# Optimization experiments

Measured on AMD Instinct MI355X. Metric: run time of the kernel, lower is better.

Reference implementation:

```python
import jax, jax.numpy as jnp
import numpy as np

DIM = 384
HEADS = 8
HEAD_DIM = DIM // HEADS
TEM_LEN = 400
SCALE = HEAD_DIM ** -0.5


def setup_inputs() -> dict:
    key = jax.random.key(0)
    ks = jax.random.split(key, 12)
    B, Lq, Lkv = 16, 1024, 1424
    inp = {
        'tem_mask': jax.random.normal(ks[0], (B, TEM_LEN, DIM), jnp.float32),
        'search_mask': jax.random.normal(ks[1], (B, Lkv - TEM_LEN, DIM), jnp.float32),
        'q': jax.random.normal(ks[2], (B, Lq, DIM), jnp.float32),
        'kv': jax.random.normal(ks[3], (B, Lkv, DIM), jnp.float32),
        'attn_pos': jax.random.normal(ks[4], (1, HEADS, Lq, Lkv), jnp.float32),
        # learned params (attn_pos_encoding_only=True: q, fused kv, proj)
        'q_w': jax.random.normal(ks[5], (DIM, DIM), jnp.float32) * 0.02,
        'q_b': jnp.zeros((DIM,), jnp.float32),
        'kv_w': jax.random.normal(ks[6], (2 * DIM, DIM), jnp.float32) * 0.02,
        'kv_b': jnp.zeros((2 * DIM,), jnp.float32),
        'proj_w': jax.random.normal(ks[7], (DIM, DIM), jnp.float32) * 0.02,
        'proj_b': jnp.zeros((DIM,), jnp.float32),
    }
    return inp


def reference(tem_mask, search_mask, q, kv, attn_pos, q_w, q_b, kv_w, kv_b, proj_w, proj_b):
    B, Lq, C = q.shape
    Lkv = kv.shape[1]
    # projections
    qh = (q @ q_w.T + q_b).reshape(B, Lq, HEADS, HEAD_DIM).transpose(0, 2, 1, 3)  # (B,H,Lq,hd)
    kvp = kv @ kv_w.T + kv_b                                                      # (B,Lkv,2C)
    k = kvp[..., :C]
    v = kvp[..., C:]
    # additive masks on v before head split (template tokens first, then search)
    v = jnp.concatenate([v[:, :TEM_LEN] + tem_mask, v[:, TEM_LEN:] + search_mask], axis=1)
    kh = k.reshape(B, Lkv, HEADS, HEAD_DIM).transpose(0, 2, 1, 3)  # (B,H,Lkv,hd)
    vh = v.reshape(B, Lkv, HEADS, HEAD_DIM).transpose(0, 2, 1, 3)  # (B,H,Lkv,hd)
    # scaled scores + untied positional bias, softmax over keys
    attn = jnp.einsum('bhqd,bhkd->bhqk', qh, kh) * SCALE + attn_pos
    attn = jax.nn.softmax(attn, axis=-1)
    x = jnp.einsum('bhqk,bhkd->bhqd', attn, vh)
    x = x.transpose(0, 2, 1, 3).reshape(B, Lq, C)
    return x @ proj_w.T + proj_b
```

## Files before the change

kernel.cpp:

```cpp
#include <hip/hip_runtime.h>
#include <stdint.h>

#define NB 16
#define NH 8
#define LQ 1024
#define LKV 1424
#define LKVP 1472
#define DIMC 384
#define NKVT 23
#define TEM 400
#define QSCALE 0.20823509f
#define LOG2E_F 1.4426950408889634f

typedef __attribute__((ext_vector_type(4))) float f32x4;
typedef __attribute__((ext_vector_type(8))) short bf16x8;
typedef __attribute__((ext_vector_type(4))) unsigned short us4;
typedef __attribute__((ext_vector_type(2))) unsigned int u32x2;
typedef __attribute__((ext_vector_type(4))) unsigned int u32x4;

__device__ __forceinline__ unsigned short f2b(float f) {
  unsigned int u = __builtin_bit_cast(unsigned int, f);
  u += 0x7fffu + ((u >> 16) & 1u);
  return (unsigned short)(u >> 16);
}

__device__ __forceinline__ void gload_lds16(const void* gsrc, void* ldst) {
  __builtin_amdgcn_global_load_lds(
      (const __attribute__((address_space(1))) void*)gsrc,
      (__attribute__((address_space(3))) void*)ldst, 16, 0, 0);
}

__global__ __launch_bounds__(256) void prep_all(
    const float* __restrict__ q, const float* __restrict__ kv,
    const float* __restrict__ qw, const float* __restrict__ kvw,
    const float* __restrict__ pw, const float* __restrict__ pos,
    unsigned short* __restrict__ qb, unsigned short* __restrict__ kvb,
    unsigned short* __restrict__ qwb, unsigned short* __restrict__ kvwb,
    unsigned short* __restrict__ pwb, unsigned short* __restrict__ Qp,
    unsigned short* __restrict__ Kp, unsigned short* __restrict__ Vt,
    unsigned short* __restrict__ posb) {
  __shared__ float lds[4][1024];
  const int bid = blockIdx.x;
  if (bid < 7632) {
    int i = bid * 256 + threadIdx.x;
    const float* src;
    unsigned short* dst;
    if (i < 16384 * 48) { src = q; dst = qb; }
    else if (i < 39168 * 48) { i -= 16384 * 48; src = kv; dst = kvb; }
    else if (i < 39552 * 48) { i -= 39168 * 48; src = qw; dst = qwb; }
    else if (i < 40320 * 48) { i -= 39552 * 48; src = kvw; dst = kvwb; }
    else { i -= 40320 * 48; src = pw; dst = pwb; }
    int row = i / 48, ch = i - row * 48;
    const float* sp = src + (size_t)row * DIMC + ch * 8;
    f32x4 x = *(const f32x4*)sp;
    f32x4 y = *(const f32x4*)(sp + 4);
    bf16x8 o;
    o[0] = (short)f2b(x[0]); o[1] = (short)f2b(x[1]);
    o[2] = (short)f2b(x[2]); o[3] = (short)f2b(x[3]);
    o[4] = (short)f2b(y[0]); o[5] = (short)f2b(y[1]);
    o[6] = (short)f2b(y[2]); o[7] = (short)f2b(y[3]);
    int blk = ch >> 3, c3 = (ch & 7) ^ (row & 7);
    *(bf16x8*)(dst + (size_t)row * DIMC + blk * 64 + c3 * 8) = o;
  } else if (bid < 9024) {
    int i = (bid - 7632) * 256 + threadIdx.x;
    u32x4 z = {0u, 0u, 0u, 0u};
    if (i < 131072) {
      *(u32x4*)(Qp + (size_t)i * 64 + 48) = z;
      *(u32x4*)(Qp + (size_t)i * 64 + 56) = z;
    } else if (i < 131072 + 188416) {
      int r = i - 131072;
      int s = r % LKVP;
      unsigned short* row = Kp + (size_t)r * 64;
      if (s < LKV) {
        *(u32x4*)(row + (6 ^ (s & 7)) * 8) = z;
        *(u32x4*)(row + (7 ^ (s & 7)) * 8) = z;
      } else {
#pragma unroll
        for (int c = 0; c < 64; c += 8) *(u32x4*)(row + c) = z;
      }
    } else if (i < 131072 + 188416 + 36864) {
      int j = i - 319488;
      int row = j / 6, x = 2 + j - (j / 6) * 6;
      int d = row % 48;
      *(u32x4*)(Vt + (size_t)row * LKVP + 1408 + ((x ^ d) & 7) * 8) = z;
    }
  } else {
    const int r = bid - 9024;
    const int q16 = r & 63, h = r >> 6;
    const int wave = threadIdx.x >> 6, lane = threadIdx.x & 63;
    const int l16 = lane & 15, g = lane >> 4;
    float* L = &lds[wave][0];
    for (int t = wave; t < NKVT; t += 4) {
#pragma unroll
      for (int i = 0; i < 4; ++i) {
        const int row = i * 4 + g;
        const int gcol = t * 64 + l16 * 4;
        f32x4 v;
        if (gcol < LKV) {
          v = *(const f32x4*)(pos + ((size_t)h * LQ + q16 * 16 + row) * LKV + gcol);
          v *= LOG2E_F;
        } else {
          f32x4 neg = {-1e30f, -1e30f, -1e30f, -1e30f};
          v = neg;
        }
        *(f32x4*)(L + row * 64 + ((l16 ^ (row & 7)) << 2)) = v;
      }
      unsigned short vals[16];
#pragma unroll
      for (int ni = 0; ni < 4; ++ni) {
        f32x4 wv = *(const f32x4*)(L + l16 * 64 + (((4 * ni + g) ^ (l16 & 7)) << 2));
#pragma unroll
        for (int rr = 0; rr < 4; ++rr) vals[4 * ni + rr] = f2b(wv[rr]);
      }
      unsigned short* op = posb + ((((size_t)h * 64 + q16) * NKVT + t) * 64 + lane) * 16;
      bf16x8 a, b;
#pragma unroll
      for (int k = 0; k < 8; ++k) { a[k] = (short)vals[k]; b[k] = (short)vals[8 + k]; }
      *(bf16x8*)op = a;
      *(bf16x8*)(op + 8) = b;
    }
  }
}

template <int MODE>
__device__ __forceinline__ void proj_body(
    unsigned short* Ash, unsigned short* Bsh, int n0, int m0,
    const unsigned short* __restrict__ A, const unsigned short* __restrict__ Wb,
    const float* __restrict__ bias, const float* __restrict__ tem,
    const float* __restrict__ srch, unsigned short* __restrict__ Oq,
    unsigned short* __restrict__ Ok, unsigned short* __restrict__ Ovt,
    float* __restrict__ Of) {
  const int tid = threadIdx.x;
  const int lane = tid & 63, l16 = lane & 15, g = lane >> 4;
  const int wave = tid >> 6, wm = wave >> 1, wn = wave & 1;

  f32x4 acc[4][4];
#pragma unroll
  for (int i = 0; i < 4; ++i)
#pragma unroll
    for (int j = 0; j < 4; ++j) { f32x4 z = {0.f, 0.f, 0.f, 0.f}; acc[i][j] = z; }

  const char* Abase = (const char*)A + (size_t)m0 * 768;
  const char* Bbase = (const char*)Wb + (size_t)n0 * 768;

  for (int ks = 0; ks < 6; ++ks) {
    __syncthreads();
#pragma unroll
    for (int rnd = 0; rnd < 4; ++rnd) {
      int idx = tid + rnd * 256;
      int row = idx >> 3, chunk = idx & 7;
      gload_lds16(Abase + (size_t)row * 768 + ks * 128 + chunk * 16,
                  (char*)Ash + idx * 16);
    }
#pragma unroll
    for (int rnd = 0; rnd < 4; ++rnd) {
      int idx = tid + rnd * 256;
      int row = idx >> 3, chunk = idx & 7;
      gload_lds16(Bbase + (size_t)row * 768 + ks * 128 + chunk * 16,
                  (char*)Bsh + idx * 16);
    }
    asm volatile("s_waitcnt vmcnt(0)" ::: "memory");
    __syncthreads();
#pragma unroll
    for (int kk = 0; kk < 2; ++kk) {
      bf16x8 a[4], bb[4];
#pragma unroll
      for (int mi = 0; mi < 4; ++mi) {
        int row = wm * 64 + mi * 16 + l16;
        a[mi] = *(const bf16x8*)((char*)Ash + row * 128 + (((g + 4 * kk) ^ (row & 7)) << 4));
      }
#pragma unroll
      for (int ni = 0; ni < 4; ++ni) {
        int row = wn * 64 + ni * 16 + l16;
        bb[ni] = *(const bf16x8*)((char*)Bsh + row * 128 + (((g + 4 * kk) ^ (row & 7)) << 4));
      }
#pragma unroll
      for (int mi = 0; mi < 4; ++mi)
#pragma unroll
        for (int ni = 0; ni < 4; ++ni)
          acc[mi][ni] = __builtin_amdgcn_mfma_f32_16x16x32_bf16(a[mi], bb[ni], acc[mi][ni], 0, 0, 0);
    }
  }

#pragma unroll
  for (int mi = 0; mi < 4; ++mi) {
    const int m_g0 = m0 + wm * 64 + mi * 16 + 4 * g;
#pragma unroll
    for (int ni = 0; ni < 4; ++ni) {
      const int n_g = n0 + wn * 64 + ni * 16 + l16;
      const float bv = bias[n_g];
      if (MODE == 0) {
        const int hh = n_g / 48, d = n_g - hh * 48;
#pragma unroll
        for (int r = 0; r < 4; ++r) {
          const int m_g = m_g0 + r;
          const int b = m_g >> 10, m = m_g & 1023;
          Oq[(((size_t)b * NH + hh) * LQ + m) * 64 + d] = f2b((acc[mi][ni][r] + bv) * QSCALE);
        }
      } else if (MODE == 2) {
#pragma unroll
        for (int r = 0; r < 4; ++r)
          Of[(size_t)(m_g0 + r) * DIMC + n_g] = acc[mi][ni][r] + bv;
      } else {
        const int b = m_g0 / LKV, s0 = m_g0 - b * LKV;
        if (n_g < DIMC) {
          const int hh = n_g / 48, d = n_g - hh * 48;
#pragma unroll
          for (int r = 0; r < 4; ++r) {
            const int s = s0 + r;
            const int dsw = (d & 7) | ((((d >> 3) ^ (s & 7)) & 7) << 3);
            Ok[(((size_t)b * NH + hh) * LKVP + s) * 64 + dsw] = f2b(acc[mi][ni][r] + bv);
          }
        } else {
          const int c = n_g - DIMC, hh = c / 48, d = c - hh * 48;
          const float* mb = (s0 < TEM)
                                ? tem + ((size_t)b * TEM + s0) * DIMC + c
                                : srch + ((size_t)b * (LKV - TEM) + (s0 - TEM)) * DIMC + c;
          const int off = s0 & 63;
          const int soff = (s0 & ~63) | ((((off >> 3) ^ d) & 7) << 3) | (off & 7);
          us4 pk;
#pragma unroll
          for (int r = 0; r < 4; ++r)
            pk[r] = f2b(acc[mi][ni][r] + bv + mb[(size_t)r * DIMC]);
          *(us4*)(Ovt + (((size_t)b * NH + hh) * 48 + d) * LKVP + soff) = pk;
        }
      }
    }
  }
}

__global__ __launch_bounds__(256) void proj_qkv(
    const unsigned short* __restrict__ qb, const unsigned short* __restrict__ qwb,
    const float* __restrict__ q_b, const unsigned short* __restrict__ kvb,
    const unsigned short* __restrict__ kvwb, const float* __restrict__ kv_b,
    const float* __restrict__ tem, const float* __restrict__ srch,
    unsigned short* __restrict__ Qp, unsigned short* __restrict__ Ok,
    unsigned short* __restrict__ Ovt) {
  __shared__ unsigned short Ash[128 * 64];
  __shared__ unsigned short Bsh[128 * 64];
  const int bid = blockIdx.x;
  if (bid < 384) {
    proj_body<0>(Ash, Bsh, (bid % 3) * 128, (bid / 3) * 128, qb, qwb, q_b,
                 nullptr, nullptr, Qp, nullptr, nullptr, nullptr);
  } else {
    const int r = bid - 384;
    proj_body<1>(Ash, Bsh, (r % 6) * 128, (r / 6) * 128, kvb, kvwb, kv_b,
                 tem, srch, nullptr, Ok, Ovt, nullptr);
  }
}

__global__ __launch_bounds__(256) void proj_out(
    const unsigned short* __restrict__ X, const unsigned short* __restrict__ pwb,
    const float* __restrict__ p_b, float* __restrict__ out) {
  __shared__ unsigned short Ash[128 * 64];
  __shared__ unsigned short Bsh[128 * 64];
  proj_body<2>(Ash, Bsh, (blockIdx.x % 3) * 128, (blockIdx.x / 3) * 128, X, pwb, p_b,
               nullptr, nullptr, nullptr, nullptr, nullptr, out);
}

__device__ __forceinline__ void stage_tile(const char* kbase, const char* vbase, int t,
                                           char* kdst, char* vdst, int wave, int lane) {
  const char* ks = kbase + (size_t)t * 8192 + wave * 2048 + lane * 16;
  char* kd = kdst + wave * 2048;
  gload_lds16(ks, kd);
  gload_lds16(ks + 1024, kd + 1024);
  if (wave < 3) {
    const char* vs = vbase + (size_t)(wave * 16 + (lane >> 3)) * (LKVP * 2) +
                     (size_t)t * 128 + (lane & 7) * 16;
    char* vd = vdst + wave * 2048;
    gload_lds16(vs, vd);
    gload_lds16(vs + 8 * (LKVP * 2), vd + 1024);
  }
}

__device__ __forceinline__ float expsum16(f32x4 (&sx)[4]) {
#pragma unroll
  for (int ni = 0; ni < 4; ++ni)
#pragma unroll
    for (int r = 0; r < 4; ++r) sx[ni][r] = exp2f(sx[ni][r]);
  float s0 = (sx[0][0] + sx[0][1]) + (sx[0][2] + sx[0][3]);
  float s1 = (sx[1][0] + sx[1][1]) + (sx[1][2] + sx[1][3]);
  float s2 = (sx[2][0] + sx[2][1]) + (sx[2][2] + sx[2][3]);
  float s3 = (sx[3][0] + sx[3][1]) + (sx[3][2] + sx[3][3]);
  float sum = (s0 + s1) + (s2 + s3);
  sum += __shfl_xor(sum, 16);
  sum += __shfl_xor(sum, 32);
  return sum;
}

__device__ __forceinline__ void packP(const f32x4 (&sx)[4], char* pbase, int swz, int g,
                                      bf16x8& af0, bf16x8& af1) {
#pragma unroll
  for (int ni = 0; ni < 4; ++ni) {
    float e0 = sx[ni][0], e1 = sx[ni][1], e2 = sx[ni][2], e3 = sx[ni][3];
    unsigned int lo, hi;
    asm("v_cvt_pk_bf16_f32 %0, %1, %2" : "=v"(lo) : "v"(e0), "v"(e1));
    asm("v_cvt_pk_bf16_f32 %0, %1, %2" : "=v"(hi) : "v"(e2), "v"(e3));
    u32x2 pk = {lo, hi};
    *(u32x2*)(pbase + ((32 * ni + 8 * g) ^ swz)) = pk;
  }
  af0 = *(const bf16x8*)(pbase + ((16 * g) ^ swz));
  af1 = *(const bf16x8*)(pbase + ((64 + 16 * g) ^ swz));
}

__device__ __forceinline__ void unpack_pos(const u32x4& w0, const u32x4& w1,
                                           f32x4 (&s)[4]) {
#pragma unroll
  for (int k = 0; k < 4; ++k) {
    const int ni = k >> 1, j2 = (k & 1) * 2;
    unsigned int a = w0[k], b = w1[k];
    s[ni][j2]         = __builtin_bit_cast(float, a << 16);
    s[ni][j2 + 1]     = __builtin_bit_cast(float, a & 0xffff0000u);
    s[ni + 2][j2]     = __builtin_bit_cast(float, b << 16);
    s[ni + 2][j2 + 1] = __builtin_bit_cast(float, b & 0xffff0000u);
  }
}

__global__ __launch_bounds__(256, 4) void attn_fwd(
    const unsigned short* __restrict__ posb, const unsigned short* __restrict__ Qp,
    const unsigned short* __restrict__ Kp, const unsigned short* __restrict__ Vt,
    unsigned short* __restrict__ X) {
  __shared__ unsigned short Ksh[2][64 * 64];
  __shared__ unsigned short Vsh[2][48 * 64];
  __shared__ unsigned short Psh[4][16 * 64];

  const int tid = threadIdx.x;
  const int lane = tid & 63, l16 = lane & 15, g = lane >> 4;
  const int wave = tid >> 6;
  const int bid = blockIdx.x;
  const int bh = bid & 127, qt = bid >> 7;
  const int b = bh >> 3, h = bh & 7;
  const int qrow = qt * 128 + wave * 32;

  bf16x8 qf[2][2];
#pragma unroll
  for (int qs = 0; qs < 2; ++qs) {
    const unsigned short* qb = Qp + ((size_t)bh * LQ + qrow + qs * 16 + l16) * 64 + 8 * g;
    qf[qs][0] = *(const bf16x8*)qb;
    qf[qs][1] = *(const bf16x8*)(qb + 32);
  }

  float l_run0 = 0.f, l_run1 = 0.f;
  f32x4 o[2][3];
#pragma unroll
  for (int qs = 0; qs < 2; ++qs)
#pragma unroll
    for (int d = 0; d < 3; ++d) { f32x4 z = {0.f, 0.f, 0.f, 0.f}; o[qs][d] = z; }

  const char* kbase = (const char*)(Kp + (size_t)bh * LKVP * 64);
  const char* vbase = (const char*)(Vt + (size_t)bh * 48 * LKVP);
  const int q16b = qt * 8 + wave * 2;
  const unsigned short* pq0 = posb + (((size_t)h * 64 + q16b) * NKVT) * 1024 + lane * 16;
  const unsigned short* pq1 = pq0 + (size_t)NKVT * 1024;
  char* pbase = (char*)&Psh[wave][0] + l16 * 128;
  const int swz = (l16 & 7) << 4;

  stage_tile(kbase, vbase, 0, (char*)&Ksh[0][0], (char*)&Vsh[0][0], wave, lane);
  asm volatile("s_waitcnt vmcnt(0)" ::: "memory");
  __syncthreads();

  int buf = 0;
  for (int t = 0; t < NKVT; ++t) {
    if (t + 1 < NKVT)
      stage_tile(kbase, vbase, t + 1, (char*)&Ksh[buf ^ 1][0], (char*)&Vsh[buf ^ 1][0],
                 wave, lane);

    u32x4 w0 = *(const u32x4*)(pq0);
    u32x4 w1 = *(const u32x4*)(pq0 + 8);
    u32x4 w2 = *(const u32x4*)(pq1);
    u32x4 w3 = *(const u32x4*)(pq1 + 8);
    pq0 += 1024; pq1 += 1024;

    f32x4 s0[4], s1[4];
    unpack_pos(w0, w1, s0);
    unpack_pos(w2, w3, s1);

#pragma unroll
    for (int ni = 0; ni < 4; ++ni) {
      const int krow = ni * 16 + l16;
      const char* kr = (const char*)&Ksh[buf][0] + krow * 128;
      bf16x8 kf0 = *(const bf16x8*)(kr + ((g ^ (krow & 7)) << 4));
      bf16x8 kf1 = *(const bf16x8*)(kr + (((g + 4) ^ (krow & 7)) << 4));
      s0[ni] = __builtin_amdgcn_mfma_f32_16x16x32_bf16(kf0, qf[0][0], s0[ni], 0, 0, 0);
      s0[ni] = __builtin_amdgcn_mfma_f32_16x16x32_bf16(kf1, qf[0][1], s0[ni], 0, 0, 0);
      s1[ni] = __builtin_amdgcn_mfma_f32_16x16x32_bf16(kf0, qf[1][0], s1[ni], 0, 0, 0);
      s1[ni] = __builtin_amdgcn_mfma_f32_16x16x32_bf16(kf1, qf[1][1], s1[ni], 0, 0, 0);
    }

    l_run0 += expsum16(s0);
    bf16x8 af00, af01, af10, af11;
    packP(s0, pbase, swz, g, af00, af01);
    l_run1 += expsum16(s1);
#pragma unroll
    for (int dn = 0; dn < 3; ++dn) {
      const int vr = 16 * dn + l16;
      const char* vrp = (const char*)&Vsh[buf][0] + vr * 128;
      bf16x8 vf0 = *(const bf16x8*)(vrp + ((g ^ (vr & 7)) << 4));
      bf16x8 vf1 = *(const bf16x8*)(vrp + (((g + 4) ^ (vr & 7)) << 4));
      o[0][dn] = __builtin_amdgcn_mfma_f32_16x16x32_bf16(af00, vf0, o[0][dn], 0, 0, 0);
      o[0][dn] = __builtin_amdgcn_mfma_f32_16x16x32_bf16(af01, vf1, o[0][dn], 0, 0, 0);
    }
    packP(s1, pbase, swz, g, af10, af11);
#pragma unroll
    for (int dn = 0; dn < 3; ++dn) {
      const int vr = 16 * dn + l16;
      const char* vrp = (const char*)&Vsh[buf][0] + vr * 128;
      bf16x8 vf0 = *(const bf16x8*)(vrp + ((g ^ (vr & 7)) << 4));
      bf16x8 vf1 = *(const bf16x8*)(vrp + (((g + 4) ^ (vr & 7)) << 4));
      o[1][dn] = __builtin_amdgcn_mfma_f32_16x16x32_bf16(af10, vf0, o[1][dn], 0, 0, 0);
      o[1][dn] = __builtin_amdgcn_mfma_f32_16x16x32_bf16(af11, vf1, o[1][dn], 0, 0, 0);
    }

    asm volatile("s_waitcnt vmcnt(0)" ::: "memory");
    __syncthreads();
    buf ^= 1;
  }

#pragma unroll
  for (int qs = 0; qs < 2; ++qs) {
    const float linv = 1.f / (qs == 0 ? l_run0 : l_run1);
#pragma unroll
    for (int r = 0; r < 4; ++r) {
      const float ib = __shfl(linv, 4 * (lane >> 4) + r);
      const int m = qrow + qs * 16 + 4 * g + r;
#pragma unroll
      for (int dn = 0; dn < 3; ++dn) {
        const int c = h * 48 + 16 * dn + l16;
        const int cs = (c & ~63) | (c & 7) | ((((c >> 3) & 7) ^ (m & 7)) << 3);
        const f32x4& ov = (qs == 0) ? o[0][dn] : o[1][dn];
        X[((size_t)b * LQ + m) * DIMC + cs] = f2b(ov[r] * ib);
      }
    }
  }
}

extern "C" void kernel_launch(void* const* d_in, const int* in_sizes, int n_in,
                              void* d_out, int out_size, void* d_ws, size_t ws_size,
                              hipStream_t stream) {
  const float* tem  = (const float*)d_in[0];
  const float* srch = (const float*)d_in[1];
  const float* q    = (const float*)d_in[2];
  const float* kv   = (const float*)d_in[3];
  const float* pos  = (const float*)d_in[4];
  const float* q_w  = (const float*)d_in[5];
  const float* q_b  = (const float*)d_in[6];
  const float* kv_w = (const float*)d_in[7];
  const float* kv_b = (const float*)d_in[8];
  const float* p_w  = (const float*)d_in[9];
  const float* p_b  = (const float*)d_in[10];
  float* out = (float*)d_out;

  char* w = (char*)d_ws;
  unsigned short* Qp   = (unsigned short*)(w);
  unsigned short* Kp   = (unsigned short*)(w + 16777216);
  unsigned short* Vt   = (unsigned short*)(w + 40894464);
  unsigned short* X    = (unsigned short*)(w + 58982400);
  unsigned short* qb   = X;
  unsigned short* posb = (unsigned short*)(w + 71565312);
  unsigned short* kvb  = (unsigned short*)(w + 95682560);
  unsigned short* qwb  = (unsigned short*)(w + 113180672);
  unsigned short* kvwb = (unsigned short*)(w + 113475584);
  unsigned short* pwb  = (unsigned short*)(w + 114065408);

  prep_all<<<9536, 256, 0, stream>>>(q, kv, q_w, kv_w, p_w, pos, qb, kvb, qwb, kvwb,
                                     pwb, Qp, Kp, Vt, posb);
  proj_qkv<<<1452, 256, 0, stream>>>(qb, qwb, q_b, kvb, kvwb, kv_b, tem, srch,
                                     Qp, Kp, Vt);
  attn_fwd<<<1024, 256, 0, stream>>>(posb, Qp, Kp, Vt, X);
  proj_out<<<384, 256, 0, stream>>>(X, pwb, p_b, out);
}
```

Baseline: 209.8 us.

## Compute softmax row sums via MFMA with ones and prefetch positional bias

Replaces the per-tile VALU reduction and cross-lane shuffles for the softmax denominator with extra MFMAs that multiply the packed bf16 probabilities by a ones vector, accumulating row sums in matrix-core registers. It also software-pipelines the positional-bias global loads one tile ahead so their latency overlaps the current tile's compute. The row sums now come from bf16-rounded probabilities, which matches the numerator's precision. In exchange it adds four MFMAs per tile and keeps more registers live.

```diff
diff --git a/kernel.cpp b/kernel.cpp
--- a/kernel.cpp
+++ b/kernel.cpp
@@ -273,19 +273,11 @@
   }
 }
 
-__device__ __forceinline__ float expsum16(f32x4 (&sx)[4]) {
+__device__ __forceinline__ void exp16(f32x4 (&sx)[4]) {
 #pragma unroll
   for (int ni = 0; ni < 4; ++ni)
 #pragma unroll
     for (int r = 0; r < 4; ++r) sx[ni][r] = exp2f(sx[ni][r]);
-  float s0 = (sx[0][0] + sx[0][1]) + (sx[0][2] + sx[0][3]);
-  float s1 = (sx[1][0] + sx[1][1]) + (sx[1][2] + sx[1][3]);
-  float s2 = (sx[2][0] + sx[2][1]) + (sx[2][2] + sx[2][3]);
-  float s3 = (sx[3][0] + sx[3][1]) + (sx[3][2] + sx[3][3]);
-  float sum = (s0 + s1) + (s2 + s3);
-  sum += __shfl_xor(sum, 16);
-  sum += __shfl_xor(sum, 32);
-  return sum;
 }
 
 __device__ __forceinline__ void packP(const f32x4 (&sx)[4], char* pbase, int swz, int g,
@@ -340,12 +332,19 @@
     qf[qs][1] = *(const bf16x8*)(qb + 32);
   }
 
-  float l_run0 = 0.f, l_run1 = 0.f;
+  bf16x8 ones;
+#pragma unroll
+  for (int i = 0; i < 8; ++i) ones[i] = (short)0x3F80;
+
+  f32x4 lsum[2];
   f32x4 o[2][3];
 #pragma unroll
-  for (int qs = 0; qs < 2; ++qs)
-#pragma unroll
-    for (int d = 0; d < 3; ++d) { f32x4 z = {0.f, 0.f, 0.f, 0.f}; o[qs][d] = z; }
+  for (int qs = 0; qs < 2; ++qs) {
+    f32x4 z = {0.f, 0.f, 0.f, 0.f};
+    lsum[qs] = z;
+#pragma unroll
+    for (int d = 0; d < 3; ++d) o[qs][d] = z;
+  }
 
   const char* kbase = (const char*)(Kp + (size_t)bh * LKVP * 64);
   const char* vbase = (const char*)(Vt + (size_t)bh * 48 * LKVP);
@@ -356,6 +355,13 @@
   const int swz = (l16 & 7) << 4;
 
   stage_tile(kbase, vbase, 0, (char*)&Ksh[0][0], (char*)&Vsh[0][0], wave, lane);
+
+  u32x4 w0 = *(const u32x4*)(pq0);
+  u32x4 w1 = *(const u32x4*)(pq0 + 8);
+  u32x4 w2 = *(const u32x4*)(pq1);
+  u32x4 w3 = *(const u32x4*)(pq1 + 8);
+  pq0 += 1024; pq1 += 1024;
+
   asm volatile("s_waitcnt vmcnt(0)" ::: "memory");
   __syncthreads();
 
@@ -365,15 +371,16 @@
       stage_tile(kbase, vbase, t + 1, (char*)&Ksh[buf ^ 1][0], (char*)&Vsh[buf ^ 1][0],
                  wave, lane);
 
-    u32x4 w0 = *(const u32x4*)(pq0);
-    u32x4 w1 = *(const u32x4*)(pq0 + 8);
-    u32x4 w2 = *(const u32x4*)(pq1);
-    u32x4 w3 = *(const u32x4*)(pq1 + 8);
-    pq0 += 1024; pq1 += 1024;
-
     f32x4 s0[4], s1[4];
     unpack_pos(w0, w1, s0);
     unpack_pos(w2, w3, s1);
+    if (t + 1 < NKVT) {
+      w0 = *(const u32x4*)(pq0);
+      w1 = *(const u32x4*)(pq0 + 8);
+      w2 = *(const u32x4*)(pq1);
+      w3 = *(const u32x4*)(pq1 + 8);
+      pq0 += 1024; pq1 += 1024;
+    }
 
 #pragma unroll
     for (int ni = 0; ni < 4; ++ni) {
@@ -387,10 +394,10 @@
       s1[ni] = __builtin_amdgcn_mfma_f32_16x16x32_bf16(kf1, qf[1][1], s1[ni], 0, 0, 0);
     }
 
-    l_run0 += expsum16(s0);
+    exp16(s0);
     bf16x8 af00, af01, af10, af11;
     packP(s0, pbase, swz, g, af00, af01);
-    l_run1 += expsum16(s1);
+    exp16(s1);
 #pragma unroll
     for (int dn = 0; dn < 3; ++dn) {
       const int vr = 16 * dn + l16;
@@ -400,6 +407,8 @@
       o[0][dn] = __builtin_amdgcn_mfma_f32_16x16x32_bf16(af00, vf0, o[0][dn], 0, 0, 0);
       o[0][dn] = __builtin_amdgcn_mfma_f32_16x16x32_bf16(af01, vf1, o[0][dn], 0, 0, 0);
     }
+    lsum[0] = __builtin_amdgcn_mfma_f32_16x16x32_bf16(af00, ones, lsum[0], 0, 0, 0);
+    lsum[0] = __builtin_amdgcn_mfma_f32_16x16x32_bf16(af01, ones, lsum[0], 0, 0, 0);
     packP(s1, pbase, swz, g, af10, af11);
 #pragma unroll
     for (int dn = 0; dn < 3; ++dn) {
@@ -410,6 +419,8 @@
       o[1][dn] = __builtin_amdgcn_mfma_f32_16x16x32_bf16(af10, vf0, o[1][dn], 0, 0, 0);
       o[1][dn] = __builtin_amdgcn_mfma_f32_16x16x32_bf16(af11, vf1, o[1][dn], 0, 0, 0);
     }
+    lsum[1] = __builtin_amdgcn_mfma_f32_16x16x32_bf16(af10, ones, lsum[1], 0, 0, 0);
+    lsum[1] = __builtin_amdgcn_mfma_f32_16x16x32_bf16(af11, ones, lsum[1], 0, 0, 0);
 
     asm volatile("s_waitcnt vmcnt(0)" ::: "memory");
     __syncthreads();
@@ -418,17 +429,15 @@
 
 #pragma unroll
   for (int qs = 0; qs < 2; ++qs) {
-    const float linv = 1.f / (qs == 0 ? l_run0 : l_run1);
 #pragma unroll
     for (int r = 0; r < 4; ++r) {
-      const float ib = __shfl(linv, 4 * (lane >> 4) + r);
+      const float ib = 1.f / lsum[qs][r];
       const int m = qrow + qs * 16 + 4 * g + r;
 #pragma unroll
       for (int dn = 0; dn < 3; ++dn) {
         const int c = h * 48 + 16 * dn + l16;
         const int cs = (c & ~63) | (c & 7) | ((((c >> 3) & 7) ^ (m & 7)) << 3);
-        const f32x4& ov = (qs == 0) ? o[0][dn] : o[1][dn];
-        X[((size_t)b * LQ + m) * DIMC + cs] = f2b(ov[r] * ib);
+        X[((size_t)b * LQ + m) * DIMC + cs] = f2b(o[qs][dn][r] * ib);
       }
     }
   }
```

Measured after the change: 205.3 us. 2.1% less time.
